# Optimization experiments

Measured on AMD Instinct MI355X. Metric: run time of the kernel, lower is better.

## Reference

```python
import jax, jax.numpy as jnp
import numpy as np

B, H, T, D = 2, 16, 2048, 64
R1, R2 = 4, 8


def setup_inputs() -> dict:
    key = jax.random.key(0)
    ks = jax.random.split(key, 7)
    return {
        "q": jax.random.normal(ks[0], (B, H, T, D), dtype=jnp.float32),
        "k": jax.random.normal(ks[1], (B, H, T, D), dtype=jnp.float32),
        "v": jax.random.normal(ks[2], (B, H, T, D), dtype=jnp.float32),
        "W_q": jax.random.normal(ks[3], (H, D, R1 * R2), dtype=jnp.float32) / np.sqrt(D),
        "W_k": jax.random.normal(ks[4], (H, D, R1 * R2), dtype=jnp.float32) / np.sqrt(D),
        "core1": jax.random.normal(ks[5], (H, R1), dtype=jnp.float32),
        "core2": jax.random.normal(ks[6], (H, R2), dtype=jnp.float32),
    }


def reference(q, k, v, W_q, W_k, core1, core2):
    """Kronecker low-rank (LSR) causal attention.

    scores[b,h,m,n] = (1/sqrt(R1*R2)) * sum_r kron[h,r] * (q@W_q)[b,h,m,r] * (k@W_k)[b,h,n,r]
    where kron[h] = core1[h] (x) core2[h]  (per-head Kronecker product).
    """
    Hh, r1 = core1.shape
    r2 = core2.shape[1]
    # per-head Kronecker core vector: (H, R1*R2)
    kron = (core1[:, :, None] * core2[:, None, :]).reshape(Hh, r1 * r2)
    scale = 1.0 / jnp.sqrt(jnp.float32(r1 * r2))
    # low-rank projections, rank R = R1*R2
    q_lr = jnp.einsum("bhtd,hdr->bhtr", q, W_q) * kron[None, :, None, :]  # [B,H,T,R]
    k_lr = jnp.einsum("bhtd,hdr->bhtr", k, W_k)                            # [B,H,T,R]
    scores = jnp.einsum("bhmr,bhnr->bhmn", q_lr, k_lr) * scale             # [B,H,T,T]
    t = q.shape[2]
    causal = jnp.tril(jnp.ones((t, t), dtype=bool))
    scores = jnp.where(causal[None, None], scores, -jnp.inf)
    p = jax.nn.softmax(scores, axis=-1)
    return jnp.einsum("bhmn,bhnd->bhmd", p, v)
```

## Files before the change

### kernel.cpp

```cpp
#include <hip/hip_runtime.h>

typedef _Float16 f16;
typedef _Float16 f16x2 __attribute__((ext_vector_type(2)));
typedef _Float16 f16x4 __attribute__((ext_vector_type(4)));
typedef _Float16 f16x8 __attribute__((ext_vector_type(8)));
typedef float    f32x4 __attribute__((ext_vector_type(4)));
typedef float    f32x16 __attribute__((ext_vector_type(16)));

constexpr int B_ = 2, H_ = 16, T_ = 2048, D_ = 64, R_ = 32, NT = 32;
constexpr int NROW = B_ * H_ * T_;

__device__ __forceinline__ f32x4 mfma16(f16x8 a, f16x8 b, f32x4 c) {
  return __builtin_amdgcn_mfma_f32_16x16x32_f16(a, b, c, 0, 0, 0);
}
__device__ __forceinline__ f32x16 mfma32(f16x8 a, f16x8 b, f32x16 c) {
  return __builtin_amdgcn_mfma_f32_32x32x16_f16(a, b, c, 0, 0, 0);
}
__device__ __forceinline__ void ld_lds16(const void* g, void* l) {
  __builtin_amdgcn_global_load_lds(
      (const __attribute__((address_space(1))) unsigned int*)g,
      (__attribute__((address_space(3))) unsigned int*)l, 16, 0, 0);
}

__global__ __launch_bounds__(256) void proj_kernel(
    const float* __restrict__ q, const float* __restrict__ k, const float* __restrict__ v,
    const float* __restrict__ Wq, const float* __restrict__ Wk,
    const float* __restrict__ c1, const float* __restrict__ c2,
    f16* __restrict__ qlr, f16* __restrict__ klr, f16* __restrict__ vt)
{
  __shared__ float sv[64 * 65];

  const int tid = threadIdx.x, w = tid >> 6, lane = tid & 63;
  const int l15 = lane & 15, l4 = lane >> 4;
  const int bh = blockIdx.x >> 5, h = bh & (H_ - 1);
  const int t0 = (blockIdx.x & 31) * 64;

  const float* vb = v + ((size_t)bh * T_ + t0) * D_;
  float4 vld[4];
#pragma unroll
  for (int it = 0; it < 4; ++it) vld[it] = ((const float4*)vb)[it * 256 + tid];

  const int m = t0 + 16 * w + l15;
  const float* qr = q + ((size_t)bh * T_ + m) * D_;
  const float* kr = k + ((size_t)bh * T_ + m) * D_;
  f16x8 aq[2], ak[2];
#pragma unroll
  for (int kc = 0; kc < 2; ++kc) {
    float4 x0 = *(const float4*)(qr + kc * 32 + 8 * l4);
    float4 x1 = *(const float4*)(qr + kc * 32 + 8 * l4 + 4);
    float4 y0 = *(const float4*)(kr + kc * 32 + 8 * l4);
    float4 y1 = *(const float4*)(kr + kc * 32 + 8 * l4 + 4);
    f16x8 A, K;
    A[0]=(f16)x0.x; A[1]=(f16)x0.y; A[2]=(f16)x0.z; A[3]=(f16)x0.w;
    A[4]=(f16)x1.x; A[5]=(f16)x1.y; A[6]=(f16)x1.z; A[7]=(f16)x1.w;
    K[0]=(f16)y0.x; K[1]=(f16)y0.y; K[2]=(f16)y0.z; K[3]=(f16)y0.w;
    K[4]=(f16)y1.x; K[5]=(f16)y1.y; K[6]=(f16)y1.z; K[7]=(f16)y1.w;
    aq[kc] = A; ak[kc] = K;
  }

  const float* Wqh = Wq + (size_t)h * D_ * R_;
  const float* Wkh = Wk + (size_t)h * D_ * R_;
  f16x8 bq[2][2], bk[2][2];
#pragma unroll
  for (int kc = 0; kc < 2; ++kc)
#pragma unroll
    for (int nt = 0; nt < 2; ++nt) {
      const int r = 16 * nt + l15;
      f16x8 q8, k8;
#pragma unroll
      for (int j2 = 0; j2 < 8; ++j2) {
        const int d = kc * 32 + 8 * l4 + j2;
        q8[j2] = (f16)Wqh[d * R_ + r];
        k8[j2] = (f16)Wkh[d * R_ + r];
      }
      bq[kc][nt] = q8; bk[kc][nt] = k8;
    }

#pragma unroll
  for (int it = 0; it < 4; ++it) {
    const int i4 = it * 256 + tid, t = i4 >> 4, dq = (i4 & 15) * 4;
    sv[t * 65 + dq    ] = vld[it].x;
    sv[t * 65 + dq + 1] = vld[it].y;
    sv[t * 65 + dq + 2] = vld[it].z;
    sv[t * 65 + dq + 3] = vld[it].w;
  }

  const f32x4 z4 = {0.f, 0.f, 0.f, 0.f};
#pragma unroll
  for (int nt = 0; nt < 2; ++nt) {
    f32x4 accq = mfma16(aq[0], bq[0][nt], z4);
    accq = mfma16(aq[1], bq[1][nt], accq);
    f32x4 acck = mfma16(ak[0], bk[0][nt], z4);
    acck = mfma16(ak[1], bk[1][nt], acck);
    const int r = 16 * nt + l15;
    const float scl = c1[h * 4 + (r >> 3)] * c2[h * 8 + (r & 7)] *
                      (0.17677669529663687f * 1.4426950408889634f);
#pragma unroll
    for (int i = 0; i < 4; ++i) {
      const size_t row = (size_t)bh * T_ + t0 + 16 * w + 4 * l4 + i;
      qlr[row * R_ + r] = (f16)(accq[i] * scl);
      klr[row * R_ + r] = (f16)acck[i];
    }
  }

  __syncthreads();
#pragma unroll
  for (int it = 0; it < 8; ++it) {
    const int idx = it * 256 + tid, d = idx >> 5, t = (idx & 31) * 2;
    const float f0 = sv[t * 65 + d], f1 = sv[t * 65 + 65 + d];
    f16x2 pr; pr[0] = (f16)f0; pr[1] = (f16)f1;
    const int sw = ((((t >> 3) ^ (d & 7)) << 3) | (t & 7));
    *(f16x2*)(vt + ((size_t)bh * D_ + d) * T_ + t0 + sw) = pr;
  }
}

__global__ __launch_bounds__(128) void attn_kernel(
    const f16* __restrict__ qlr, const f16* __restrict__ klr,
    const f16* __restrict__ vt, f16* __restrict__ On, float2* __restrict__ ml,
    const int NS)
{
  __shared__ __align__(16) f16 s_k[64 * 32];
  __shared__ __align__(16) f16 s_vt[64 * 64];
  __shared__ __align__(16) f16 s_p[2][32 * 64];

  const int tid = threadIdx.x, w = tid >> 6, lane = tid & 63;
  const int l15 = lane & 15, l4 = lane >> 4, l31 = lane & 31, hh = lane >> 5;
  const int bh = blockIdx.x & 31;
  const int rest = blockIdx.x >> 5;
  const int mt = 31 - ((NS == 2) ? (rest >> 1) : rest);
  const int s  = rest & (NS - 1);
  const int m0 = mt * 64;

  const f16x8 aq0 = *(const f16x8*)(qlr + ((size_t)bh * T_ + m0 + 32 * w + l15) * R_ + 8 * l4);
  const f16x8 aq1 = *(const f16x8*)(qlr + ((size_t)bh * T_ + m0 + 32 * w + 16 + l15) * R_ + 8 * l4);

  const f16* kb = klr + (size_t)bh * T_ * R_;
  const f16* vb = vt + (size_t)bh * D_ * T_;

  f32x16 oacc[2];
#pragma unroll
  for (int c = 0; c < 2; ++c)
#pragma unroll
    for (int e = 0; e < 16; ++e) oacc[c][e] = 0.f;
  float mi0 = -1e30f, mi1 = -1e30f, li0 = 0.f, li1 = 0.f;
  const f32x4 z4 = {0.f, 0.f, 0.f, 0.f};

  for (int j = s; j <= mt; j += NS) {
    const int n0 = 64 * j;
    __syncthreads();
#pragma unroll
    for (int e = 0; e < 2; ++e)
      ld_lds16((const char*)kb + (size_t)n0 * 64 + (2 * w + e) * 1024 + lane * 16,
               (char*)s_k + (2 * w + e) * 1024);
#pragma unroll
    for (int e = 0; e < 4; ++e) {
      const int d0 = w * 32 + e * 8;
      ld_lds16((const char*)vb + ((size_t)(d0 + (lane >> 3)) * T_ + n0) * 2 + (lane & 7) * 16,
               (char*)s_vt + d0 * 128);
    }
    __syncthreads();

    f32x4 sc[4][2];
#pragma unroll
    for (int ns = 0; ns < 4; ++ns) {
      f16x8 akf = *(const f16x8*)&s_k[(16 * ns + l15) * 32 + 8 * l4];
      sc[ns][0] = mfma16(akf, aq0, z4);
      sc[ns][1] = mfma16(akf, aq1, z4);
    }
    if (j == mt) {
      const int lim0 = 32 * w + l15;
#pragma unroll
      for (int ns = 0; ns < 4; ++ns) {
        const int nb = 16 * ns + 4 * l4;
#pragma unroll
        for (int i = 0; i < 4; ++i) {
          if (nb + i > lim0)      sc[ns][0][i] = -1e30f;
          if (nb + i > lim0 + 16) sc[ns][1][i] = -1e30f;
        }
      }
    }

    float rm0 = -1e30f, rm1 = -1e30f;
#pragma unroll
    for (int ns = 0; ns < 4; ++ns)
#pragma unroll
      for (int i = 0; i < 4; ++i) {
        rm0 = fmaxf(rm0, sc[ns][0][i]);
        rm1 = fmaxf(rm1, sc[ns][1][i]);
      }
    rm0 = fmaxf(rm0, __shfl_xor(rm0, 16)); rm0 = fmaxf(rm0, __shfl_xor(rm0, 32));
    rm1 = fmaxf(rm1, __shfl_xor(rm1, 16)); rm1 = fmaxf(rm1, __shfl_xor(rm1, 32));
    const float mn0 = fmaxf(mi0, rm0), mn1 = fmaxf(mi1, rm1);
    const float a0 = exp2f(mi0 - mn0), a1 = exp2f(mi1 - mn1);
    float rs0 = 0.f, rs1 = 0.f;
#pragma unroll
    for (int ns = 0; ns < 4; ++ns) {
      f16x4 p0v, p1v;
#pragma unroll
      for (int i = 0; i < 4; ++i) {
        const float p0 = exp2f(sc[ns][0][i] - mn0);
        const float p1 = exp2f(sc[ns][1][i] - mn1);
        rs0 += p0; rs1 += p1;
        p0v[i] = (f16)p0; p1v[i] = (f16)p1;
      }
      const int col = ((((2 * ns + (l4 >> 1)) ^ (l15 & 7)) << 3) | (4 * (l4 & 1)));
      *(f16x4*)&s_p[w][l15 * 64 + col]        = p0v;
      *(f16x4*)&s_p[w][(16 + l15) * 64 + col] = p1v;
    }
    rs0 += __shfl_xor(rs0, 16); rs0 += __shfl_xor(rs0, 32);
    rs1 += __shfl_xor(rs1, 16); rs1 += __shfl_xor(rs1, 32);
    li0 = li0 * a0 + rs0; li1 = li1 * a1 + rs1;
    mi0 = mn0; mi1 = mn1;
    const float aPV = (lane & 16) ? a1 : a0;
#pragma unroll
    for (int c = 0; c < 2; ++c) oacc[c] *= aPV;

#pragma unroll
    for (int kc = 0; kc < 4; ++kc) {
      const int u = (2 * kc + hh) ^ (l31 & 7);
      f16x8 bp = *(const f16x8*)&s_p[w][l31 * 64 + u * 8];
#pragma unroll
      for (int c = 0; c < 2; ++c) {
        f16x8 av = *(const f16x8*)&s_vt[(32 * c + l31) * 64 + u * 8];
        oacc[c] = mfma32(av, bp, oacc[c]);
      }
    }
  }

  const float myl = (lane & 16) ? li1 : li0;
  const float invl = myl > 0.f ? 1.f / myl : 0.f;
  f16* ob = On + (((size_t)s * 32 + bh) * T_ + m0 + 32 * w + l31) * D_;
#pragma unroll
  for (int c = 0; c < 2; ++c)
#pragma unroll
    for (int g = 0; g < 4; ++g) {
      f16x4 o;
#pragma unroll
      for (int e = 0; e < 4; ++e) o[e] = (f16)(oacc[c][4 * g + e] * invl);
      *(f16x4*)(ob + 32 * c + 8 * g + 4 * hh) = o;
    }
  if (l4 < 2) {
    float2 mlv;
    mlv.x = l4 ? mi1 : mi0;
    mlv.y = l4 ? li1 : li0;
    ml[((size_t)s * 32 + bh) * T_ + m0 + 32 * w + 16 * l4 + l15] = mlv;
  }
}

__global__ __launch_bounds__(256) void merge_kernel(
    const f16* __restrict__ On, const float2* __restrict__ ml,
    float* __restrict__ out, const int NS)
{
  const int row = blockIdx.x * 32 + (threadIdx.x >> 3);
  const int d0 = (threadIdx.x & 7) * 8;
  const f16x8 o0 = *(const f16x8*)(On + (size_t)row * 64 + d0);
  float res[8];
  if (NS == 2) {
    const float2 a = ml[row];
    const float2 b = ml[NROW + row];
    const f16x8 o1 = *(const f16x8*)(On + ((size_t)NROW + row) * 64 + d0);
    const float ms = fmaxf(a.x, b.x);
    const float w0 = exp2f(a.x - ms) * a.y;
    const float w1 = exp2f(b.x - ms) * b.y;
    const float inv = 1.f / (w0 + w1);
    const float c0 = w0 * inv, c1 = w1 * inv;
#pragma unroll
    for (int e = 0; e < 8; ++e) res[e] = c0 * (float)o0[e] + c1 * (float)o1[e];
  } else {
#pragma unroll
    for (int e = 0; e < 8; ++e) res[e] = (float)o0[e];
  }
  float* ob = out + (size_t)row * 64 + d0;
  f32x4 r0, r1;
#pragma unroll
  for (int e = 0; e < 4; ++e) { r0[e] = res[e]; r1[e] = res[4 + e]; }
  *(f32x4*)ob = r0;
  *(f32x4*)(ob + 4) = r1;
}

extern "C" void kernel_launch(void* const* d_in, const int* in_sizes, int n_in,
                              void* d_out, int out_size, void* d_ws, size_t ws_size,
                              hipStream_t stream) {
  const float* q  = (const float*)d_in[0];
  const float* k  = (const float*)d_in[1];
  const float* v  = (const float*)d_in[2];
  const float* Wq = (const float*)d_in[3];
  const float* Wk = (const float*)d_in[4];
  const float* c1 = (const float*)d_in[5];
  const float* c2 = (const float*)d_in[6];
  float* out = (float*)d_out;

  f16* qlr = (f16*)d_ws;
  f16* klr = qlr + (size_t)B_ * H_ * T_ * R_;
  f16* vt  = klr + (size_t)B_ * H_ * T_ * R_;
  f16* On  = vt + (size_t)B_ * H_ * T_ * D_;
  float2* ml = (float2*)(On + (size_t)2 * NROW * D_);

  const int NS = (ws_size >= ((size_t)33 * 1024 * 1024 + (1 << 20))) ? 2 : 1;

  proj_kernel<<<B_ * H_ * NT, 256, 0, stream>>>(q, k, v, Wq, Wk, c1, c2, qlr, klr, vt);
  attn_kernel<<<B_ * H_ * NT * NS, 128, 0, stream>>>(qlr, klr, vt, On, ml, NS);
  merge_kernel<<<NROW / 32, 256, 0, stream>>>(On, ml, out, NS);
}
```

Before: 153.6 us.

## Pair complementary causal query tiles per block and double-buffer K/V staging

Each block now handles two query tiles, pr and 31-pr, so every block does the same total causal work and the K/V tiles loaded into LDS are reused by both tiles. K and V^T staging is double-buffered so the next tile's global-to-LDS load is issued before the current tile is computed, which also drops one barrier per iteration. The grid is halved. The cost is more registers from two sets of accumulators and twice the LDS, which may lower occupancy.

```diff
diff --git a/kernel.cpp b/kernel.cpp
--- a/kernel.cpp
+++ b/kernel.cpp
@@ -114,137 +114,176 @@
   }
 }
 
+
+__device__ __forceinline__ void compute_tile(
+    const f16* __restrict__ sk, const f16* __restrict__ svt, f16* __restrict__ sp,
+    const f16x8 aq0, const f16x8 aq1, const bool diag,
+    float& mi0, float& mi1, float& li0, float& li1, f32x16* oacc,
+    const int w, const int lane)
+{
+  const int l15 = lane & 15, l4 = lane >> 4, l31 = lane & 31, hh = lane >> 5;
+  const f32x4 z4 = {0.f, 0.f, 0.f, 0.f};
+
+  f32x4 sc[4][2];
+#pragma unroll
+  for (int ns = 0; ns < 4; ++ns) {
+    f16x8 akf = *(const f16x8*)&sk[(16 * ns + l15) * 32 + 8 * l4];
+    sc[ns][0] = mfma16(akf, aq0, z4);
+    sc[ns][1] = mfma16(akf, aq1, z4);
+  }
+  if (diag) {
+    const int lim0 = 32 * w + l15;
+#pragma unroll
+    for (int ns = 0; ns < 4; ++ns) {
+      const int nb = 16 * ns + 4 * l4;
+#pragma unroll
+      for (int i = 0; i < 4; ++i) {
+        if (nb + i > lim0)      sc[ns][0][i] = -1e30f;
+        if (nb + i > lim0 + 16) sc[ns][1][i] = -1e30f;
+      }
+    }
+  }
+
+  float rm0 = -1e30f, rm1 = -1e30f;
+#pragma unroll
+  for (int ns = 0; ns < 4; ++ns)
+#pragma unroll
+    for (int i = 0; i < 4; ++i) {
+      rm0 = fmaxf(rm0, sc[ns][0][i]);
+      rm1 = fmaxf(rm1, sc[ns][1][i]);
+    }
+  rm0 = fmaxf(rm0, __shfl_xor(rm0, 16)); rm0 = fmaxf(rm0, __shfl_xor(rm0, 32));
+  rm1 = fmaxf(rm1, __shfl_xor(rm1, 16)); rm1 = fmaxf(rm1, __shfl_xor(rm1, 32));
+  const float mn0 = fmaxf(mi0, rm0), mn1 = fmaxf(mi1, rm1);
+  const float a0 = exp2f(mi0 - mn0), a1 = exp2f(mi1 - mn1);
+  float rs0 = 0.f, rs1 = 0.f;
+#pragma unroll
+  for (int ns = 0; ns < 4; ++ns) {
+    f16x4 p0v, p1v;
+#pragma unroll
+    for (int i = 0; i < 4; ++i) {
+      const float p0 = exp2f(sc[ns][0][i] - mn0);
+      const float p1 = exp2f(sc[ns][1][i] - mn1);
+      rs0 += p0; rs1 += p1;
+      p0v[i] = (f16)p0; p1v[i] = (f16)p1;
+    }
+    const int col = ((((2 * ns + (l4 >> 1)) ^ (l15 & 7)) << 3) | (4 * (l4 & 1)));
+    *(f16x4*)&sp[l15 * 64 + col]        = p0v;
+    *(f16x4*)&sp[(16 + l15) * 64 + col] = p1v;
+  }
+  rs0 += __shfl_xor(rs0, 16); rs0 += __shfl_xor(rs0, 32);
+  rs1 += __shfl_xor(rs1, 16); rs1 += __shfl_xor(rs1, 32);
+  li0 = li0 * a0 + rs0; li1 = li1 * a1 + rs1;
+  mi0 = mn0; mi1 = mn1;
+  const float aPV = (lane & 16) ? a1 : a0;
+#pragma unroll
+  for (int c = 0; c < 2; ++c) oacc[c] *= aPV;
+
+#pragma unroll
+  for (int kc = 0; kc < 4; ++kc) {
+    const int u = (2 * kc + hh) ^ (l31 & 7);
+    f16x8 bp = *(const f16x8*)&sp[l31 * 64 + u * 8];
+#pragma unroll
+    for (int c = 0; c < 2; ++c) {
+      f16x8 av = *(const f16x8*)&svt[(32 * c + l31) * 64 + u * 8];
+      oacc[c] = mfma32(av, bp, oacc[c]);
+    }
+  }
+}
+
+__device__ __forceinline__ void write_out(
+    f16* __restrict__ On, float2* __restrict__ ml, const size_t base,
+    const f32x16* oacc, const float mi0, const float mi1,
+    const float li0, const float li1, const int w, const int lane)
+{
+  const int l15 = lane & 15, l4 = lane >> 4, l31 = lane & 31, hh = lane >> 5;
+  const float myl = (lane & 16) ? li1 : li0;
+  const float invl = myl > 0.f ? 1.f / myl : 0.f;
+  f16* ob = On + (base + 32 * w + l31) * D_;
+#pragma unroll
+  for (int c = 0; c < 2; ++c)
+#pragma unroll
+    for (int g = 0; g < 4; ++g) {
+      f16x4 o;
+#pragma unroll
+      for (int e = 0; e < 4; ++e) o[e] = (f16)(oacc[c][4 * g + e] * invl);
+      *(f16x4*)(ob + 32 * c + 8 * g + 4 * hh) = o;
+    }
+  if (l4 < 2) {
+    float2 mlv;
+    mlv.x = l4 ? mi1 : mi0;
+    mlv.y = l4 ? li1 : li0;
+    ml[base + 32 * w + 16 * l4 + l15] = mlv;
+  }
+}
+
 __global__ __launch_bounds__(128) void attn_kernel(
     const f16* __restrict__ qlr, const f16* __restrict__ klr,
     const f16* __restrict__ vt, f16* __restrict__ On, float2* __restrict__ ml,
     const int NS)
 {
-  __shared__ __align__(16) f16 s_k[64 * 32];
-  __shared__ __align__(16) f16 s_vt[64 * 64];
+  __shared__ __align__(16) f16 s_k[2][64 * 32];
+  __shared__ __align__(16) f16 s_vt[2][64 * 64];
   __shared__ __align__(16) f16 s_p[2][32 * 64];
 
   const int tid = threadIdx.x, w = tid >> 6, lane = tid & 63;
-  const int l15 = lane & 15, l4 = lane >> 4, l31 = lane & 31, hh = lane >> 5;
+  const int l15 = lane & 15, l4 = lane >> 4;
   const int bh = blockIdx.x & 31;
   const int rest = blockIdx.x >> 5;
-  const int mt = 31 - ((NS == 2) ? (rest >> 1) : rest);
   const int s  = rest & (NS - 1);
-  const int m0 = mt * 64;
-
-  const f16x8 aq0 = *(const f16x8*)(qlr + ((size_t)bh * T_ + m0 + 32 * w + l15) * R_ + 8 * l4);
-  const f16x8 aq1 = *(const f16x8*)(qlr + ((size_t)bh * T_ + m0 + 32 * w + 16 + l15) * R_ + 8 * l4);
+  const int pr = (NS == 2) ? (rest >> 1) : rest;
+  const int mtA = pr, mtB = 31 - pr;
+  const int m0A = mtA * 64, m0B = mtB * 64;
+
+  const f16x8 aqA0 = *(const f16x8*)(qlr + ((size_t)bh * T_ + m0A + 32 * w + l15) * R_ + 8 * l4);
+  const f16x8 aqA1 = *(const f16x8*)(qlr + ((size_t)bh * T_ + m0A + 32 * w + 16 + l15) * R_ + 8 * l4);
+  const f16x8 aqB0 = *(const f16x8*)(qlr + ((size_t)bh * T_ + m0B + 32 * w + l15) * R_ + 8 * l4);
+  const f16x8 aqB1 = *(const f16x8*)(qlr + ((size_t)bh * T_ + m0B + 32 * w + 16 + l15) * R_ + 8 * l4);
 
   const f16* kb = klr + (size_t)bh * T_ * R_;
   const f16* vb = vt + (size_t)bh * D_ * T_;
 
-  f32x16 oacc[2];
+  f32x16 oA[2], oB[2];
 #pragma unroll
   for (int c = 0; c < 2; ++c)
 #pragma unroll
-    for (int e = 0; e < 16; ++e) oacc[c][e] = 0.f;
-  float mi0 = -1e30f, mi1 = -1e30f, li0 = 0.f, li1 = 0.f;
-  const f32x4 z4 = {0.f, 0.f, 0.f, 0.f};
-
-  for (int j = s; j <= mt; j += NS) {
+    for (int e = 0; e < 16; ++e) { oA[c][e] = 0.f; oB[c][e] = 0.f; }
+  float miA0 = -1e30f, miA1 = -1e30f, liA0 = 0.f, liA1 = 0.f;
+  float miB0 = -1e30f, miB1 = -1e30f, liB0 = 0.f, liB1 = 0.f;
+
+  auto stage = [&](int bf, int j) {
     const int n0 = 64 * j;
-    __syncthreads();
 #pragma unroll
     for (int e = 0; e < 2; ++e)
       ld_lds16((const char*)kb + (size_t)n0 * 64 + (2 * w + e) * 1024 + lane * 16,
-               (char*)s_k + (2 * w + e) * 1024);
+               (char*)(&s_k[bf][0]) + (2 * w + e) * 1024);
 #pragma unroll
     for (int e = 0; e < 4; ++e) {
       const int d0 = w * 32 + e * 8;
       ld_lds16((const char*)vb + ((size_t)(d0 + (lane >> 3)) * T_ + n0) * 2 + (lane & 7) * 16,
-               (char*)s_vt + d0 * 128);
-    }
+               (char*)(&s_vt[bf][0]) + d0 * 128);
+    }
+  };
+
+  stage(0, s);
+  __syncthreads();
+  int buf = 0;
+  for (int j = s; j <= mtB; j += NS) {
+    const int jn = j + NS;
+    if (jn <= mtB) stage(buf ^ 1, jn);
+    if (j <= mtA)
+      compute_tile(&s_k[buf][0], &s_vt[buf][0], &s_p[w][0], aqA0, aqA1, j == mtA,
+                   miA0, miA1, liA0, liA1, oA, w, lane);
+    compute_tile(&s_k[buf][0], &s_vt[buf][0], &s_p[w][0], aqB0, aqB1, j == mtB,
+                 miB0, miB1, liB0, liB1, oB, w, lane);
     __syncthreads();
-
-    f32x4 sc[4][2];
-#pragma unroll
-    for (int ns = 0; ns < 4; ++ns) {
-      f16x8 akf = *(const f16x8*)&s_k[(16 * ns + l15) * 32 + 8 * l4];
-      sc[ns][0] = mfma16(akf, aq0, z4);
-      sc[ns][1] = mfma16(akf, aq1, z4);
-    }
-    if (j == mt) {
-      const int lim0 = 32 * w + l15;
-#pragma unroll
-      for (int ns = 0; ns < 4; ++ns) {
-        const int nb = 16 * ns + 4 * l4;
-#pragma unroll
-        for (int i = 0; i < 4; ++i) {
-          if (nb + i > lim0)      sc[ns][0][i] = -1e30f;
-          if (nb + i > lim0 + 16) sc[ns][1][i] = -1e30f;
-        }
-      }
-    }
-
-    float rm0 = -1e30f, rm1 = -1e30f;
-#pragma unroll
-    for (int ns = 0; ns < 4; ++ns)
-#pragma unroll
-      for (int i = 0; i < 4; ++i) {
-        rm0 = fmaxf(rm0, sc[ns][0][i]);
-        rm1 = fmaxf(rm1, sc[ns][1][i]);
-      }
-    rm0 = fmaxf(rm0, __shfl_xor(rm0, 16)); rm0 = fmaxf(rm0, __shfl_xor(rm0, 32));
-    rm1 = fmaxf(rm1, __shfl_xor(rm1, 16)); rm1 = fmaxf(rm1, __shfl_xor(rm1, 32));
-    const float mn0 = fmaxf(mi0, rm0), mn1 = fmaxf(mi1, rm1);
-    const float a0 = exp2f(mi0 - mn0), a1 = exp2f(mi1 - mn1);
-    float rs0 = 0.f, rs1 = 0.f;
-#pragma unroll
-    for (int ns = 0; ns < 4; ++ns) {
-      f16x4 p0v, p1v;
-#pragma unroll
-      for (int i = 0; i < 4; ++i) {
-        const float p0 = exp2f(sc[ns][0][i] - mn0);
-        const float p1 = exp2f(sc[ns][1][i] - mn1);
-        rs0 += p0; rs1 += p1;
-        p0v[i] = (f16)p0; p1v[i] = (f16)p1;
-      }
-      const int col = ((((2 * ns + (l4 >> 1)) ^ (l15 & 7)) << 3) | (4 * (l4 & 1)));
-      *(f16x4*)&s_p[w][l15 * 64 + col]        = p0v;
-      *(f16x4*)&s_p[w][(16 + l15) * 64 + col] = p1v;
-    }
-    rs0 += __shfl_xor(rs0, 16); rs0 += __shfl_xor(rs0, 32);
-    rs1 += __shfl_xor(rs1, 16); rs1 += __shfl_xor(rs1, 32);
-    li0 = li0 * a0 + rs0; li1 = li1 * a1 + rs1;
-    mi0 = mn0; mi1 = mn1;
-    const float aPV = (lane & 16) ? a1 : a0;
-#pragma unroll
-    for (int c = 0; c < 2; ++c) oacc[c] *= aPV;
-
-#pragma unroll
-    for (int kc = 0; kc < 4; ++kc) {
-      const int u = (2 * kc + hh) ^ (l31 & 7);
-      f16x8 bp = *(const f16x8*)&s_p[w][l31 * 64 + u * 8];
-#pragma unroll
-      for (int c = 0; c < 2; ++c) {
-        f16x8 av = *(const f16x8*)&s_vt[(32 * c + l31) * 64 + u * 8];
-        oacc[c] = mfma32(av, bp, oacc[c]);
-      }
-    }
-  }
-
-  const float myl = (lane & 16) ? li1 : li0;
-  const float invl = myl > 0.f ? 1.f / myl : 0.f;
-  f16* ob = On + (((size_t)s * 32 + bh) * T_ + m0 + 32 * w + l31) * D_;
-#pragma unroll
-  for (int c = 0; c < 2; ++c)
-#pragma unroll
-    for (int g = 0; g < 4; ++g) {
-      f16x4 o;
-#pragma unroll
-      for (int e = 0; e < 4; ++e) o[e] = (f16)(oacc[c][4 * g + e] * invl);
-      *(f16x4*)(ob + 32 * c + 8 * g + 4 * hh) = o;
-    }
-  if (l4 < 2) {
-    float2 mlv;
-    mlv.x = l4 ? mi1 : mi0;
-    mlv.y = l4 ? li1 : li0;
-    ml[((size_t)s * 32 + bh) * T_ + m0 + 32 * w + 16 * l4 + l15] = mlv;
-  }
+    buf ^= 1;
+  }
+
+  const size_t baseA = ((size_t)s * 32 + bh) * T_ + m0A;
+  const size_t baseB = ((size_t)s * 32 + bh) * T_ + m0B;
+  write_out(On, ml, baseA, oA, miA0, miA1, liA0, liA1, w, lane);
+  write_out(On, ml, baseB, oB, miB0, miB1, liB0, liB1, w, lane);
 }
 
 __global__ __launch_bounds__(256) void merge_kernel(
@@ -299,6 +338,6 @@
   const int NS = (ws_size >= ((size_t)33 * 1024 * 1024 + (1 << 20))) ? 2 : 1;
 
   proj_kernel<<<B_ * H_ * NT, 256, 0, stream>>>(q, k, v, Wq, Wk, c1, c2, qlr, klr, vt);
-  attn_kernel<<<B_ * H_ * NT * NS, 128, 0, stream>>>(qlr, klr, vt, On, ml, NS);
+  attn_kernel<<<32 * 16 * NS, 128, 0, stream>>>(qlr, klr, vt, On, ml, NS);
   merge_kernel<<<NROW / 32, 256, 0, stream>>>(On, ml, out, NS);
 }
```

Result: no change. 154.4 us (+0.5%).
